# Kernel tuning notes

Hardware: AMD Instinct MI355X
Metric: run time of the kernel (lower is better)

## Reference

```python
import jax, jax.numpy as jnp
import numpy as np

T, B, C, H, W = 5, 32, 32, 64, 64
V_TH = 0.5
GAMMA = 0.5
E_EXC = 1.5
E_INH = -0.5
G_LEAK_BASE = 0.7
LOWER = 0.5   # target_rate - rate_margin
UPPER = 0.7   # target_rate + rate_margin


@jax.custom_vjp
def spike_fn(x):
    # heaviside forward, rectangular surrogate gradient backward
    return (x >= 0).astype(x.dtype)

def _spike_fwd(x):
    return spike_fn(x), x

def _spike_bwd(x, g):
    return (g * jnp.clip(GAMMA - jnp.abs(x), 0.0, None) / (GAMMA * GAMMA),)

spike_fn.defvjp(_spike_fwd, _spike_bwd)


def setup_inputs() -> dict:
    key = jax.random.key(0)
    k1, k2 = jax.random.split(key)
    x_exc = jax.random.uniform(k1, (T, B, C, H, W), dtype=jnp.float32)
    x_inh = jax.random.uniform(k2, (T, B, C, H, W), dtype=jnp.float32)
    tau_param = jnp.zeros((C, 1, 1), dtype=jnp.float32)  # nn.Parameter init
    return {"x_exc": x_exc, "x_inh": x_inh, "tau_param": tau_param}


def reference(x_exc, x_inh, tau_param):
    # dt_tau: [C,1,1] broadcasts against [B,C,H,W] state
    dt_tau = jnp.clip(jax.nn.sigmoid(tau_param), 0.05, 1.0)

    mem0 = jnp.zeros_like(x_exc[0])
    ema0 = jnp.zeros_like(mem0)
    gmod0 = jnp.zeros_like(mem0)

    def step(carry, g_t):
        mem, ema, gmod = carry
        g_exc, g_inh = g_t
        current_leak_g = jnp.clip(G_LEAK_BASE - gmod, 0.01, 1.0)
        d_mem = (g_exc * (E_EXC - mem)
                 + g_inh * (E_INH - mem)
                 + current_leak_g * (-mem)) * dt_tau
        mem = mem + d_mem
        s = spike_fn(mem - V_TH)
        ema = 0.5 * ema + 0.5 * jax.lax.stop_gradient(s)
        # original skips this update at t == T-1, but gmod is only read at
        # the NEXT step, so updating unconditionally yields identical output
        weight = 2.0 * (jax.nn.sigmoid(LOWER - ema) - jax.nn.sigmoid(ema - UPPER))
        gmod = 0.9 * gmod + 0.1 * weight
        mem = mem - V_TH * s  # soft reset
        return (mem, ema, gmod), s

    _, spikes = jax.lax.scan(step, (mem0, ema0, gmod0), (x_exc, x_inh))
    return spikes  # [T, B, C, H, W]
```

## Files before the change

### kernel.cpp

```cpp
#include <hip/hip_runtime.h>


#define N_T 5
#define N_ELEM (32 * 32 * 64 * 64)
#define N_VEC (N_ELEM / 4)
#define HW4   (64 * 64 / 4)

__device__ __forceinline__ float sigf(float x) {
    return 1.0f / (1.0f + expf(-x));
}

__global__ __launch_bounds__(256) void lif_fwd(
    const float4* __restrict__ xe,
    const float4* __restrict__ xi,
    const float*  __restrict__ tau,
    float4*       __restrict__ out)
{
    const int i = blockIdx.x * 256 + threadIdx.x;
    const int c = (i / HW4) & 31;
    float dt = 1.0f / (1.0f + expf(-tau[c]));
    dt = fminf(fmaxf(dt, 0.05f), 1.0f);

    float m[4]   = {0.f, 0.f, 0.f, 0.f};
    float ema[4] = {0.f, 0.f, 0.f, 0.f};
    float gm[4]  = {0.f, 0.f, 0.f, 0.f};

#pragma unroll
    for (int t = 0; t < N_T; ++t) {
        const float4 ge4 = xe[t * N_VEC + i];
        const float4 gi4 = xi[t * N_VEC + i];
        const float ge[4] = {ge4.x, ge4.y, ge4.z, ge4.w};
        const float gi[4] = {gi4.x, gi4.y, gi4.z, gi4.w};
        float s[4];
#pragma unroll
        for (int k = 0; k < 4; ++k) {
            float leak = fminf(fmaxf(0.7f - gm[k], 0.01f), 1.0f);
            float mm = m[k];
            float d  = (ge[k] * (1.5f - mm) + gi[k] * (-0.5f - mm) + leak * (-mm)) * dt;
            mm += d;
            float sv = (mm - 0.5f >= 0.0f) ? 1.0f : 0.0f;
            ema[k] = 0.5f * ema[k] + 0.5f * sv;
            float w = 2.0f * (sigf(0.5f - ema[k]) - sigf(ema[k] - 0.7f));
            gm[k] = 0.9f * gm[k] + 0.1f * w;
            m[k]  = mm - 0.5f * sv;
            s[k]  = sv;
        }
        out[t * N_VEC + i] = make_float4(s[0], s[1], s[2], s[3]);
    }
}

extern "C" void kernel_launch(void* const* d_in, const int* in_sizes, int n_in,
                              void* d_out, int out_size, void* d_ws, size_t ws_size,
                              hipStream_t stream) {
    const float4* xe  = (const float4*)d_in[0];
    const float4* xi  = (const float4*)d_in[1];
    const float*  tau = (const float*)d_in[2];
    float4* out = (float4*)d_out;
    lif_fwd<<<N_VEC / 256, 256, 0, stream>>>(xe, xi, tau, out);
}
```

Measured before the change: 44.04 us.

## Replace per-element adaptation sigmoids with spike-history lookup table and nontemporal stores

Since ema and gmod depend only on the binary spike history, each block precomputes the leak conductance for all 31 possible history prefixes into a shared-memory table. Each element then tracks a tree node index and looks up its leak instead of evaluating two sigmoids per step. Output spikes are written with nontemporal stores to avoid polluting cache. This adds a small per-block setup and a __syncthreads, and LDS lookups with divergent indices.

```diff
diff --git a/kernel.cpp b/kernel.cpp
--- a/kernel.cpp
+++ b/kernel.cpp
@@ -1,10 +1,12 @@
 #include <hip/hip_runtime.h>
 
 
-#define N_T 5
+#define N_T   5
 #define N_ELEM (32 * 32 * 64 * 64)
-#define N_VEC (N_ELEM / 4)
-#define HW4   (64 * 64 / 4)
+#define N_VEC  (N_ELEM / 4)
+#define HW4    (64 * 64 / 4)
+
+typedef float v4f __attribute__((ext_vector_type(4)));
 
 __device__ __forceinline__ float sigf(float x) {
     return 1.0f / (1.0f + expf(-x));
@@ -14,16 +16,31 @@
     const float4* __restrict__ xe,
     const float4* __restrict__ xi,
     const float*  __restrict__ tau,
-    float4*       __restrict__ out)
+    float*        __restrict__ out)
 {
-    const int i = blockIdx.x * 256 + threadIdx.x;
+    __shared__ float lut[32];
+    const int tid = threadIdx.x;
+    if (tid < 31) {
+        unsigned v = tid + 1u;
+        int d = 31 - __builtin_clz(v);
+        float ema = 0.0f, gm = 0.0f;
+        for (int b = d - 1; b >= 0; --b) {
+            float s = (float)((v >> b) & 1u);
+            ema = 0.5f * ema + 0.5f * s;
+            float w = 2.0f * (sigf(0.5f - ema) - sigf(ema - 0.7f));
+            gm = 0.9f * gm + 0.1f * w;
+        }
+        lut[tid] = fminf(fmaxf(0.7f - gm, 0.01f), 1.0f);
+    }
+    __syncthreads();
+
+    const int i = blockIdx.x * 256 + tid;
     const int c = (i / HW4) & 31;
-    float dt = 1.0f / (1.0f + expf(-tau[c]));
+    float dt = sigf(tau[c]);
     dt = fminf(fmaxf(dt, 0.05f), 1.0f);
 
-    float m[4]   = {0.f, 0.f, 0.f, 0.f};
-    float ema[4] = {0.f, 0.f, 0.f, 0.f};
-    float gm[4]  = {0.f, 0.f, 0.f, 0.f};
+    float m[4]    = {0.f, 0.f, 0.f, 0.f};
+    int   node[4] = {0, 0, 0, 0};
 
 #pragma unroll
     for (int t = 0; t < N_T; ++t) {
@@ -34,18 +51,16 @@
         float s[4];
 #pragma unroll
         for (int k = 0; k < 4; ++k) {
-            float leak = fminf(fmaxf(0.7f - gm[k], 0.01f), 1.0f);
+            float leak = lut[node[k]];
             float mm = m[k];
-            float d  = (ge[k] * (1.5f - mm) + gi[k] * (-0.5f - mm) + leak * (-mm)) * dt;
-            mm += d;
+            mm += (ge[k] * (1.5f - mm) + gi[k] * (-0.5f - mm) + leak * (-mm)) * dt;
             float sv = (mm - 0.5f >= 0.0f) ? 1.0f : 0.0f;
-            ema[k] = 0.5f * ema[k] + 0.5f * sv;
-            float w = 2.0f * (sigf(0.5f - ema[k]) - sigf(ema[k] - 0.7f));
-            gm[k] = 0.9f * gm[k] + 0.1f * w;
-            m[k]  = mm - 0.5f * sv;
-            s[k]  = sv;
+            node[k] = 2 * node[k] + 1 + (int)sv;
+            m[k] = mm - 0.5f * sv;
+            s[k] = sv;
         }
-        out[t * N_VEC + i] = make_float4(s[0], s[1], s[2], s[3]);
+        v4f o = {s[0], s[1], s[2], s[3]};
+        __builtin_nontemporal_store(o, (v4f*)&out[4 * (t * N_VEC + i)]);
     }
 }
 
@@ -55,6 +70,6 @@
     const float4* xe  = (const float4*)d_in[0];
     const float4* xi  = (const float4*)d_in[1];
     const float*  tau = (const float*)d_in[2];
-    float4* out = (float4*)d_out;
+    float* out = (float*)d_out;
     lif_fwd<<<N_VEC / 256, 256, 0, stream>>>(xe, xi, tau, out);
 }
```

New measurement: 41.92 us. 1.05x faster.
